# Performance work log

Hardware: AMD Instinct MI355X
Metric: run time of the kernel (lower is better)

## Reference

```python
import jax, jax.numpy as jnp
import numpy as np

NARROW = 127.0                      # narrow int8 range [-127, 127]
ACT_SCALE = 6.0 / 127.0             # fixed stand-in for learned ActQuant per-tensor scale
FLOW_SCALE = 3.96875 / 127.0        # ConstFlowQuant: max_val 3.96875, 8-bit narrow


def ste_round(x):
    # straight-through rounding (Brevitas-style)
    return x + jax.lax.stop_gradient(jnp.round(x) - x)


def act_quant(x, scale):
    # per-tensor narrow int8 fake-quant (quantize -> clamp -> dequantize)
    return scale * jnp.clip(ste_round(x / scale), -NARROW, NARROW)


def weight_quant(w):
    # per-tensor stats-based narrow int8 weight fake-quant
    s = jax.lax.stop_gradient(jnp.max(jnp.abs(w))) / NARROW + 1e-12
    return s * jnp.clip(ste_round(w / s), -NARROW, NARROW)


def conv2d(x, w, b, groups=1, pad=0):
    y = jax.lax.conv_general_dilated(
        x, w, window_strides=(1, 1), padding=[(pad, pad), (pad, pad)],
        dimension_numbers=("NCHW", "OIHW", "NCHW"), feature_group_count=groups)
    return y + b[None, :, None, None]


def setup_inputs() -> dict:
    key = jax.random.key(0)
    ks = jax.random.split(key, 12)
    B, H, W = 8, 120, 160
    cor_planes = 4 * (2 * 3 + 1) ** 2  # 196
    return {
        "flow": jax.random.normal(ks[0], (B, 2, H, W), jnp.float32),
        "corr": jax.random.normal(ks[1], (B, cor_planes, H, W), jnp.float32),
        "Wc1": jax.random.normal(ks[2], (96, cor_planes, 1, 1), jnp.float32) * 0.05,
        "bc1": jax.random.normal(ks[3], (96,), jnp.float32) * 0.05,
        "Wf1": jax.random.normal(ks[4], (64, 2, 1, 1), jnp.float32) * 0.05,
        "bf1": jax.random.normal(ks[5], (64,), jnp.float32) * 0.05,
        "Wf2": jax.random.normal(ks[6], (32, 64, 1, 1), jnp.float32) * 0.05,
        "bf2": jax.random.normal(ks[7], (32,), jnp.float32) * 0.05,
        "Wd": jax.random.normal(ks[8], (128, 1, 3, 3), jnp.float32) * 0.05,
        "bd": jax.random.normal(ks[9], (128,), jnp.float32) * 0.05,
        "Wp": jax.random.normal(ks[10], (80, 128, 1, 1), jnp.float32) * 0.05,
        "bp": jax.random.normal(ks[11], (80,), jnp.float32) * 0.05,
    }


def reference(flow, corr, Wc1, bc1, Wf1, bf1, Wf2, bf2, Wd, bd, Wp, bp):
    # convc1: 1x1 quant conv with output ActQuant, then ReLU
    cor = jax.nn.relu(act_quant(conv2d(corr, weight_quant(Wc1), bc1), ACT_SCALE))
    # convf1: 1x1 quant conv (no output quant), ReLU
    flo = jax.nn.relu(conv2d(flow, weight_quant(Wf1), bf1))
    # convf2: input ActQuant, 1x1 conv, output quant (shared with convc1), ReLU
    flo = jax.nn.relu(act_quant(conv2d(act_quant(flo, ACT_SCALE), weight_quant(Wf2), bf2), ACT_SCALE))
    # QuantCat with ConstFlowQuant on inputs and output -> [B,128,H,W]
    cor_flo = act_quant(
        jnp.concatenate([act_quant(cor, FLOW_SCALE), act_quant(flo, FLOW_SCALE)], axis=1),
        FLOW_SCALE)
    # depthwise 3x3 quant conv (groups=128), input ActQuant
    d = conv2d(act_quant(cor_flo, ACT_SCALE), weight_quant(Wd), bd, groups=128, pad=1)
    # pointwise 1x1 quant conv, input ActQuant, ReLU
    out = jax.nn.relu(conv2d(act_quant(d, ACT_SCALE), weight_quant(Wp), bp))
    # final QuantCat(out, flow) with ConstFlowQuant -> [B,82,H,W]
    return act_quant(
        jnp.concatenate([act_quant(out, FLOW_SCALE), act_quant(flow, FLOW_SCALE)], axis=1),
        FLOW_SCALE)
```

## Files before the change

### kernel.cpp

```cpp
#include <hip/hip_runtime.h>
#include <hip/hip_bf16.h>
#include <cstddef>

#define BB   8
#define HH   120
#define WW   160
#define HW   19200
#define NPIX 153600
#define CORC 196

#define AS_  ((float)(6.0/127.0))
#define FS_  0.03125f

#define OFF_WF1 18832
#define OFF_WF2 18960
#define OFF_WD  21008
#define OFF_WPQ_US 44320
#define CFQ_BYTE_OFF 131072

typedef __attribute__((ext_vector_type(8)))  short short8;
typedef __attribute__((ext_vector_type(4)))  float f32x4;
typedef unsigned int u32;

__device__ __forceinline__ float clip127(float x) {
    return fminf(fmaxf(x, -127.f), 127.f);
}

__device__ __forceinline__ unsigned short f2bf(float x) {
    unsigned int u = __float_as_uint(x);
    unsigned int r = (u + 0x7fffu + ((u >> 16) & 1u)) >> 16;
    return (unsigned short)r;
}

__global__ __launch_bounds__(256) void quant_weights(
    const float* __restrict__ Wc1, const float* __restrict__ Wf1,
    const float* __restrict__ Wf2, const float* __restrict__ Wd,
    const float* __restrict__ Wp,  float* __restrict__ ws)
{
    __shared__ float red[256];
    const int t = blockIdx.x;
    const float* src = (t == 0) ? Wc1 : (t == 1) ? Wf1 : (t == 2) ? Wf2 : (t == 3) ? Wd : Wp;
    const int n = (t == 0) ? 18816 : (t == 1) ? 128 : (t == 2) ? 2048 : (t == 3) ? 1152 : 10240;
    const int tid = threadIdx.x;

    float m = 0.f;
    for (int i = tid; i < n; i += 256) m = fmaxf(m, fabsf(src[i]));
    red[tid] = m;
    __syncthreads();
    for (int s = 128; s > 0; s >>= 1) {
        if (tid < s) red[tid] = fmaxf(red[tid], red[tid + s]);
        __syncthreads();
    }
    const float s = red[0] / 127.0f + 1e-12f;

    if (t == 0) {
        unsigned short* bf = (unsigned short*)ws + 32;
        for (int j = tid; j < 21504; j += 256) {
            const int e    = j & 7;
            const int l    = (j >> 3) & 63;
            const int tile = j >> 9;
            const int nt   = tile % 6;
            const int kt   = tile / 6;
            const int out  = nt * 16 + (l & 15);
            const int k    = kt * 32 + ((l >> 4) << 3) + e;
            float q = 0.f;
            if (k < 196) q = clip127(rintf(Wc1[out * 196 + k] / s));
            bf[j] = f2bf(q);
        }
        if (tid == 0) ws[2] = s;
    } else if (t == 4) {
        unsigned short* bf = (unsigned short*)ws + OFF_WPQ_US;
        for (int j = tid; j < 10240; j += 256) {
            const int e    = j & 7;
            const int l    = (j >> 3) & 63;
            const int tile = j >> 9;
            const int nt   = tile % 5;
            const int kt   = tile / 5;
            const int o    = nt * 16 + (l & 15);
            const int k    = kt * 32 + ((l >> 4) << 3) + e;
            const float q  = clip127(rintf(Wp[o * 128 + k] / s));
            bf[j] = f2bf(q);
        }
        if (tid == 0) ws[1] = s;
    } else {
        for (int i = tid; i < n; i += 256) {
            const float q = clip127(rintf(src[i] / s));
            if (t == 1) {
                ws[OFF_WF1 + i] = s * q;
            } else if (t == 2) {
                int o = i / 64, c = i % 64;
                ws[OFF_WF2 + c * 32 + o] = s * q;
            } else {
                ws[OFF_WD + i] = q;
            }
        }
        if (tid == 0 && t == 3) ws[0] = s;
    }
}

#define TSTRIDE 136
__global__ __launch_bounds__(256, 3) void k1_convc1(
    const float* __restrict__ corr, const float* __restrict__ bc1,
    const float* __restrict__ ws,   signed char* __restrict__ cfq)
{
    __shared__ __align__(1024) char smem[32768];

    const int tid = threadIdx.x;
    const int w   = tid >> 6;
    const int l   = tid & 63;
    const int p0  = blockIdx.x * 128;
    const int b   = p0 / HW;
    const int hw0 = p0 % HW;
    const float* cp = corr + (size_t)b * CORC * HW + hw0;

    const short8* Bfr = (const short8*)((const unsigned short*)ws + 32);

#define STAGE(KT, BASE)                                                               \
    {   _Pragma("unroll")                                                             \
        for (int i = 0; i < 4; ++i) {                                                 \
            const int cl = w * 8 + i * 2;                                             \
            int ch = (KT) * 32 + cl + (l >> 5);                                       \
            ch = ch < CORC ? ch : (CORC - 1);                                         \
            const char* src = (const char*)cp + (size_t)ch * (HW * 4) + ((l & 31) * 16); \
            u32* dst = (u32*)(smem + (BASE) + cl * 512);                              \
            __builtin_amdgcn_global_load_lds(                                         \
                (const __attribute__((address_space(1))) u32*)src,                    \
                (__attribute__((address_space(3))) u32*)dst, 16, 0, 0);               \
        }                                                                             }

    f32x4 a00 = {0.f,0.f,0.f,0.f}, a01 = a00, a02 = a00, a03 = a00, a04 = a00, a05 = a00;
    f32x4 a10 = a00, a11 = a00, a12 = a00, a13 = a00, a14 = a00, a15 = a00;

    STAGE(0, 0)
    STAGE(1, 16384)

    const int pixoff = (w * 32 + (l & 15)) * 4;
    const int chbase = (l >> 4) << 3;

#pragma unroll
    for (int kt = 0; kt < 7; ++kt) {
        const int base = (kt & 1) << 14;

        asm volatile("s_waitcnt vmcnt(4)" ::: "memory");
        __builtin_amdgcn_sched_barrier(0);
        __builtin_amdgcn_s_barrier();
        __builtin_amdgcn_sched_barrier(0);

        float v0[8], v1[8];
#pragma unroll
        for (int e = 0; e < 8; ++e) {
            const char* ap = smem + base + (chbase + e) * 512 + pixoff;
            v0[e] = *(const float*)ap;
            v1[e] = *(const float*)(ap + 64);
        }
        __builtin_amdgcn_sched_barrier(0);
        asm volatile("s_waitcnt lgkmcnt(0)" ::: "memory");
        __builtin_amdgcn_sched_barrier(0);
        __builtin_amdgcn_s_barrier();
        __builtin_amdgcn_sched_barrier(0);

        const short8 b0 = Bfr[(kt * 6 + 0) * 64 + l];
        const short8 b1 = Bfr[(kt * 6 + 1) * 64 + l];
        const short8 b2 = Bfr[(kt * 6 + 2) * 64 + l];
        const short8 b3 = Bfr[(kt * 6 + 3) * 64 + l];
        const short8 b4 = Bfr[(kt * 6 + 4) * 64 + l];
        const short8 b5 = Bfr[(kt * 6 + 5) * 64 + l];
        __builtin_amdgcn_sched_barrier(0);

        if (kt < 5) STAGE(kt + 2, base)
        __builtin_amdgcn_sched_barrier(0);

        short8 h0_, l0_, h1_, l1_;
#pragma unroll
        for (int e = 0; e < 8; ++e) {
            const float va = v0[e], vb = v1[e];
            const unsigned short ha = f2bf(va);
            const unsigned short hb = f2bf(vb);
            h0_[e] = (short)ha; h1_[e] = (short)hb;
            l0_[e] = (short)f2bf(va - __uint_as_float((unsigned int)ha << 16));
            l1_[e] = (short)f2bf(vb - __uint_as_float((unsigned int)hb << 16));
        }

#define MF(BB_, A0, A1)                                                          \
        A0 = __builtin_amdgcn_mfma_f32_16x16x32_bf16(l0_, BB_, A0, 0, 0, 0);     \
        A0 = __builtin_amdgcn_mfma_f32_16x16x32_bf16(h0_, BB_, A0, 0, 0, 0);     \
        A1 = __builtin_amdgcn_mfma_f32_16x16x32_bf16(l1_, BB_, A1, 0, 0, 0);     \
        A1 = __builtin_amdgcn_mfma_f32_16x16x32_bf16(h1_, BB_, A1, 0, 0, 0);
        MF(b0, a00, a10) MF(b1, a01, a11) MF(b2, a02, a12)
        MF(b3, a03, a13) MF(b4, a04, a14) MF(b5, a05, a15)
#undef MF
    }
#undef STAGE

    const float sc1 = ws[2];
    signed char* t8 = (signed char*)smem;

#define EPI(ACC, NT, TILE)                                                        \
    {   const int out = (NT) * 16 + (l & 15);                                     \
        const float bias = bc1[out];                                              \
        _Pragma("unroll")                                                         \
        for (int i = 0; i < 4; ++i) {                                             \
            const int prow = w * 32 + (TILE) * 16 + ((l >> 4) << 2) + i;          \
            float v  = fmaf(sc1, ACC[i], bias);                                   \
            float aq = AS_ * clip127(rintf(v / AS_));                             \
            float r  = fmaxf(aq, 0.f);                                            \
            float kk = fminf(rintf(r * 32.f), 127.f);                             \
            float cf = kk * FS_;                                                  \
            float q8 = clip127(rintf(cf / AS_));                                  \
            t8[out * TSTRIDE + prow] = (signed char)(int)q8;                      \
        }                                                                         }
    EPI(a00, 0, 0) EPI(a01, 1, 0) EPI(a02, 2, 0) EPI(a03, 3, 0) EPI(a04, 4, 0) EPI(a05, 5, 0)
    EPI(a10, 0, 1) EPI(a11, 1, 1) EPI(a12, 2, 1) EPI(a13, 3, 1) EPI(a14, 4, 1) EPI(a15, 5, 1)
#undef EPI
    __syncthreads();

#pragma unroll
    for (int r = 0; r < 12; ++r) {
        const int d   = r * 256 + tid;
        const int out = d >> 5;
        const int pd  = d & 31;
        const unsigned int v = *(const unsigned int*)(t8 + out * TSTRIDE + pd * 4);
        *(unsigned int*)(cfq + (size_t)(b * 128 + out) * HW + hw0 + pd * 4) = v;
    }
}

typedef __attribute__((ext_vector_type(16))) float f32x16;
__global__ __launch_bounds__(256) void k1_flo(
    const float* __restrict__ flow, const float* __restrict__ bf1,
    const float* __restrict__ bf2,  const float* __restrict__ ws,
    signed char* __restrict__ cfq)
{
    const int p  = blockIdx.x * 256 + threadIdx.x;
    const int b  = p / HW;
    const int hw = p % HW;

    const float f0 = flow[(size_t)(b * 2) * HW + hw];
    const float f1 = flow[(size_t)(b * 2 + 1) * HW + hw];

    f32x16 a2a, a2b;
#pragma unroll
    for (int j = 0; j < 16; ++j) { a2a[j] = 0.f; a2b[j] = 0.f; }

    for (int c = 0; c < 64; ++c) {
        const float w0 = ws[OFF_WF1 + 2 * c];
        const float w1 = ws[OFF_WF1 + 2 * c + 1];
        float v  = fmaf(f0, w0, fmaf(f1, w1, bf1[c]));
        float r  = fmaxf(v, 0.f);
        float af = AS_ * fminf(rintf(r / AS_), 127.f);
        const float* w2 = ws + OFF_WF2 + c * 32;
#pragma unroll
        for (int j = 0; j < 16; ++j) {
            a2a[j] = fmaf(af, w2[j],      a2a[j]);
            a2b[j] = fmaf(af, w2[16 + j], a2b[j]);
        }
    }

    signed char* op = cfq + (size_t)b * 128 * HW + (size_t)96 * HW + hw;
#define FLOEPI(ACC, BASE)                                                        \
    _Pragma("unroll")                                                            \
    for (int j = 0; j < 16; ++j) {                                               \
        const int o = (BASE) + j;                                                \
        float v  = ACC[j] + bf2[o];                                              \
        float aq = AS_ * clip127(rintf(v / AS_));                                \
        float r  = fmaxf(aq, 0.f);                                               \
        float kk = fminf(rintf(r * 32.f), 127.f);                                \
        float cf = kk * FS_;                                                     \
        float q8 = clip127(rintf(cf / AS_));                                     \
        op[(size_t)o * HW] = (signed char)(int)q8;                               \
    }
    FLOEPI(a2a, 0) FLOEPI(a2b, 16)
#undef FLOEPI
}

#define STG_STRIDE 44
__global__ __launch_bounds__(256) void k2_dwpw(
    const float* __restrict__ flow, const float* __restrict__ bd,
    const float* __restrict__ bp,   const float* __restrict__ ws,
    const signed char* __restrict__ cfq, float* __restrict__ out)
{
    __shared__ signed char stage[4 * 128 * STG_STRIDE];
    __shared__ unsigned short afrag[64 * 136];

    const int tid = threadIdx.x;
    const int bid = blockIdx.x;
    const int b   = bid / 300;
    const int rem = bid % 300;
    const int h0  = (rem / 5) * 2;
    const int w0  = (rem % 5) * 32;

    for (int j = tid; j < 5120; j += 256) {
        const int i   = j % 10;
        const int c   = (j / 10) % 128;
        const int row = j / 1280;
        const int h   = h0 - 1 + row;
        const int wb  = w0 - 4 + 4 * i;
        unsigned int v = 0u;
        if (h >= 0 && h < HH && wb >= 0 && wb <= WW - 4)
            v = *(const unsigned int*)(cfq + ((size_t)(b * 128 + c) * HW + (size_t)h * WW + wb));
        *(unsigned int*)(stage + (row * 128 + c) * STG_STRIDE + i * 4) = v;
    }
    __syncthreads();

    const int c0 = tid & 63;
    const int pg = tid >> 6;
    const float sd = ws[0], sp = ws[1];
    const float ASsd = AS_ * sd;

    float wd0[9], wd1[9];
#pragma unroll
    for (int t9 = 0; t9 < 9; ++t9) {
        wd0[t9] = ws[OFF_WD + c0 * 9 + t9];
        wd1[t9] = ws[OFF_WD + (c0 + 64) * 9 + t9];
    }
    const float bd0 = bd[c0], bd1 = bd[c0 + 64];

#pragma unroll
    for (int pp = 0; pp < 16; ++pp) {
        const int pix = pg * 16 + pp;
        const int r   = pix >> 5;
        const int col = pix & 31;
        float s0 = 0.f, s1 = 0.f;
#pragma unroll
        for (int dy = 0; dy < 3; ++dy) {
            const int rb = (r + dy) * 128;
            const int xb = 3 + col;
#pragma unroll
            for (int dd = 0; dd < 3; ++dd) {
                s0 = fmaf((float)stage[(rb + c0     ) * STG_STRIDE + xb + dd], wd0[dy * 3 + dd], s0);
                s1 = fmaf((float)stage[(rb + c0 + 64) * STG_STRIDE + xb + dd], wd1[dy * 3 + dd], s1);
            }
        }
        const float q0 = clip127(rintf(fmaf(ASsd, s0, bd0) / AS_));
        const float q1 = clip127(rintf(fmaf(ASsd, s1, bd1) / AS_));
        afrag[pix * 136 + c0]      = f2bf(q0);
        afrag[pix * 136 + c0 + 64] = f2bf(q1);
    }
    __syncthreads();

    const int wv = tid >> 6;
    const int l  = tid & 63;
    const unsigned short* A = afrag + (size_t)(wv * 16 + (l & 15)) * 136 + ((l >> 4) << 3);
    const short8* Bfr = (const short8*)((const unsigned short*)ws + OFF_WPQ_US);

    f32x4 pc0 = {0.f,0.f,0.f,0.f}, pc1 = pc0, pc2 = pc0, pc3 = pc0, pc4 = pc0;

#define PTSTEP(ACC, KT, NT)                                                      \
    {   short8 bq = Bfr[((KT) * 5 + (NT)) * 64 + l];                             \
        ACC = __builtin_amdgcn_mfma_f32_16x16x32_bf16(a_, bq, ACC, 0, 0, 0);     }
#pragma unroll
    for (int kt = 0; kt < 4; ++kt) {
        short8 a_ = *(const short8*)(A + kt * 32);
        PTSTEP(pc0, kt, 0) PTSTEP(pc1, kt, 1) PTSTEP(pc2, kt, 2)
        PTSTEP(pc3, kt, 3) PTSTEP(pc4, kt, 4)
    }
#undef PTSTEP

    const float ASsp = AS_ * sp;
    float* ob = out + (size_t)b * 82 * HW;

#define PEPI(ACC, NT)                                                            \
    {   const int o = (NT) * 16 + (l & 15);                                      \
        const float bias = bp[o];                                                \
        _Pragma("unroll")                                                        \
        for (int i = 0; i < 4; ++i) {                                            \
            const int pix = wv * 16 + ((l >> 4) << 2) + i;                       \
            const int hw  = (h0 + (pix >> 5)) * WW + w0 + (pix & 31);            \
            float v = fmaf(ASsp, ACC[i], bias);                                  \
            float r = fmaxf(v, 0.f);                                             \
            float k = fminf(rintf(r * 32.f), 127.f);                             \
            ob[(size_t)o * HW + hw] = k * FS_;                                   \
        }                                                                        }
    PEPI(pc0, 0) PEPI(pc1, 1) PEPI(pc2, 2) PEPI(pc3, 3) PEPI(pc4, 4)
#undef PEPI

    if (tid < 128) {
        const int ch  = tid >> 6;
        const int pix = tid & 63;
        const int hw  = (h0 + (pix >> 5)) * WW + w0 + (pix & 31);
        const float f = flow[(size_t)(b * 2 + ch) * HW + hw];
        const float k = clip127(rintf(f * 32.f));
        ob[(size_t)(80 + ch) * HW + hw] = k * FS_;
    }
}

extern "C" void kernel_launch(void* const* d_in, const int* in_sizes, int n_in,
                              void* d_out, int out_size, void* d_ws, size_t ws_size,
                              hipStream_t stream) {
    const float* flow = (const float*)d_in[0];
    const float* corr = (const float*)d_in[1];
    const float* Wc1  = (const float*)d_in[2];
    const float* bc1  = (const float*)d_in[3];
    const float* Wf1  = (const float*)d_in[4];
    const float* bf1  = (const float*)d_in[5];
    const float* Wf2  = (const float*)d_in[6];
    const float* bf2  = (const float*)d_in[7];
    const float* Wd   = (const float*)d_in[8];
    const float* bd   = (const float*)d_in[9];
    const float* Wp   = (const float*)d_in[10];
    const float* bp   = (const float*)d_in[11];

    float* ws = (float*)d_ws;
    signed char* cfq = (signed char*)d_ws + CFQ_BYTE_OFF;
    float* out = (float*)d_out;

    quant_weights<<<5, 256, 0, stream>>>(Wc1, Wf1, Wf2, Wd, Wp, ws);
    k1_convc1<<<NPIX / 128, 256, 0, stream>>>(corr, bc1, ws, cfq);
    k1_flo<<<NPIX / 256, 256, 0, stream>>>(flow, bf1, bf2, ws, cfq);
    k2_dwpw<<<2400, 256, 0, stream>>>(flow, bd, bp, ws, cfq, out);
}
```

Before: 158.7 us.

## Give each wave a private LDS slab in convc1 to drop block barriers

The convc1 kernel is restructured so each wave stages its own 32-pixel slab of corr channels into a private double-buffered LDS region. This removes the two per-iteration block-wide barriers and keeps only a vmcnt/lgkmcnt wait. Blocks shrink to 128 threads and 64 pixels, with half the shared memory, to raise occupancy. Block IDs are remapped with an XCD-aware swizzle so consecutive pixel tiles land on the same die. The cost is more, smaller blocks, narrower 128-byte global rows per channel, and a new barrier before the epilogue reuses LDS.

```diff
diff --git a/kernel.cpp b/kernel.cpp
--- a/kernel.cpp
+++ b/kernel.cpp
@@ -98,66 +98,52 @@
     }
 }
 
-#define TSTRIDE 136
-__global__ __launch_bounds__(256, 3) void k1_convc1(
+#define TS8 68
+__global__ __launch_bounds__(128, 4) void k1_convc1(
     const float* __restrict__ corr, const float* __restrict__ bc1,
     const float* __restrict__ ws,   signed char* __restrict__ cfq)
 {
-    __shared__ __align__(1024) char smem[32768];
-
-    const int tid = threadIdx.x;
-    const int w   = tid >> 6;
-    const int l   = tid & 63;
-    const int p0  = blockIdx.x * 128;
-    const int b   = p0 / HW;
-    const int hw0 = p0 % HW;
+    __shared__ __align__(1024) char smem[16384];
+
+    const int tid  = threadIdx.x;
+    const int w    = tid >> 6;
+    const int l    = tid & 63;
+    const int bid  = blockIdx.x;
+    const int wgid = (bid & 7) * 300 + (bid >> 3);
+    const int p0   = wgid * 64;
+    const int b    = p0 / HW;
+    const int hw0  = p0 % HW;
     const float* cp = corr + (size_t)b * CORC * HW + hw0;
 
     const short8* Bfr = (const short8*)((const unsigned short*)ws + 32);
-
-#define STAGE(KT, BASE)                                                               \
-    {   _Pragma("unroll")                                                             \
-        for (int i = 0; i < 4; ++i) {                                                 \
-            const int cl = w * 8 + i * 2;                                             \
-            int ch = (KT) * 32 + cl + (l >> 5);                                       \
-            ch = ch < CORC ? ch : (CORC - 1);                                         \
-            const char* src = (const char*)cp + (size_t)ch * (HW * 4) + ((l & 31) * 16); \
-            u32* dst = (u32*)(smem + (BASE) + cl * 512);                              \
-            __builtin_amdgcn_global_load_lds(                                         \
-                (const __attribute__((address_space(1))) u32*)src,                    \
-                (__attribute__((address_space(3))) u32*)dst, 16, 0, 0);               \
-        }                                                                             }
+    char* slab = smem + w * 8192;
+
+#define STAGE(KT)                                                                  \
+    {   char* dbase = slab + (((KT) & 1) << 12);                                   \
+        _Pragma("unroll")                                                          \
+        for (int i = 0; i < 4; ++i) {                                              \
+            int ch = (KT) * 32 + i * 8 + (l >> 3);                                 \
+            ch = ch < CORC ? ch : (CORC - 1);                                      \
+            const char* src = (const char*)cp + (size_t)ch * (HW * 4)              \
+                              + w * 128 + (l & 7) * 16;                            \
+            u32* dst = (u32*)(dbase + i * 1024);                                   \
+            __builtin_amdgcn_global_load_lds(                                      \
+                (const __attribute__((address_space(1))) u32*)src,                 \
+                (__attribute__((address_space(3))) u32*)dst, 16, 0, 0);            \
+        }                                                                          }
 
     f32x4 a00 = {0.f,0.f,0.f,0.f}, a01 = a00, a02 = a00, a03 = a00, a04 = a00, a05 = a00;
     f32x4 a10 = a00, a11 = a00, a12 = a00, a13 = a00, a14 = a00, a15 = a00;
 
-    STAGE(0, 0)
-    STAGE(1, 16384)
-
-    const int pixoff = (w * 32 + (l & 15)) * 4;
+    STAGE(0)
+    STAGE(1)
+
+    const int pixoff = (l & 15) * 4;
     const int chbase = (l >> 4) << 3;
 
 #pragma unroll
     for (int kt = 0; kt < 7; ++kt) {
-        const int base = (kt & 1) << 14;
-
-        asm volatile("s_waitcnt vmcnt(4)" ::: "memory");
-        __builtin_amdgcn_sched_barrier(0);
-        __builtin_amdgcn_s_barrier();
-        __builtin_amdgcn_sched_barrier(0);
-
-        float v0[8], v1[8];
-#pragma unroll
-        for (int e = 0; e < 8; ++e) {
-            const char* ap = smem + base + (chbase + e) * 512 + pixoff;
-            v0[e] = *(const float*)ap;
-            v1[e] = *(const float*)(ap + 64);
-        }
-        __builtin_amdgcn_sched_barrier(0);
-        asm volatile("s_waitcnt lgkmcnt(0)" ::: "memory");
-        __builtin_amdgcn_sched_barrier(0);
-        __builtin_amdgcn_s_barrier();
-        __builtin_amdgcn_sched_barrier(0);
+        const char* abase = slab + ((kt & 1) << 12);
 
         const short8 b0 = Bfr[(kt * 6 + 0) * 64 + l];
         const short8 b1 = Bfr[(kt * 6 + 1) * 64 + l];
@@ -165,9 +151,21 @@
         const short8 b3 = Bfr[(kt * 6 + 3) * 64 + l];
         const short8 b4 = Bfr[(kt * 6 + 4) * 64 + l];
         const short8 b5 = Bfr[(kt * 6 + 5) * 64 + l];
+
+        asm volatile("s_waitcnt vmcnt(10)" ::: "memory");
         __builtin_amdgcn_sched_barrier(0);
 
-        if (kt < 5) STAGE(kt + 2, base)
+        float v0[8], v1[8];
+#pragma unroll
+        for (int e = 0; e < 8; ++e) {
+            const char* ap = abase + (chbase + e) * 128 + pixoff;
+            v0[e] = *(const float*)ap;
+            v1[e] = *(const float*)(ap + 64);
+        }
+        asm volatile("s_waitcnt lgkmcnt(0)" ::: "memory");
+        __builtin_amdgcn_sched_barrier(0);
+
+        if (kt < 5) STAGE(kt + 2)
         __builtin_amdgcn_sched_barrier(0);
 
         short8 h0_, l0_, h1_, l1_;
@@ -193,6 +191,7 @@
 #undef STAGE
 
     const float sc1 = ws[2];
+    __syncthreads();
     signed char* t8 = (signed char*)smem;
 
 #define EPI(ACC, NT, TILE)                                                        \
@@ -207,7 +206,7 @@
             float kk = fminf(rintf(r * 32.f), 127.f);                             \
             float cf = kk * FS_;                                                  \
             float q8 = clip127(rintf(cf / AS_));                                  \
-            t8[out * TSTRIDE + prow] = (signed char)(int)q8;                      \
+            t8[out * TS8 + prow] = (signed char)(int)q8;                          \
         }                                                                         }
     EPI(a00, 0, 0) EPI(a01, 1, 0) EPI(a02, 2, 0) EPI(a03, 3, 0) EPI(a04, 4, 0) EPI(a05, 5, 0)
     EPI(a10, 0, 1) EPI(a11, 1, 1) EPI(a12, 2, 1) EPI(a13, 3, 1) EPI(a14, 4, 1) EPI(a15, 5, 1)
@@ -216,10 +215,10 @@
 
 #pragma unroll
     for (int r = 0; r < 12; ++r) {
-        const int d   = r * 256 + tid;
-        const int out = d >> 5;
-        const int pd  = d & 31;
-        const unsigned int v = *(const unsigned int*)(t8 + out * TSTRIDE + pd * 4);
+        const int d   = r * 128 + tid;
+        const int out = d >> 4;
+        const int pd  = d & 15;
+        const unsigned int v = *(const unsigned int*)(t8 + out * TS8 + pd * 4);
         *(unsigned int*)(cfq + (size_t)(b * 128 + out) * HW + hw0 + pd * 4) = v;
     }
 }
@@ -404,7 +403,7 @@
     float* out = (float*)d_out;
 
     quant_weights<<<5, 256, 0, stream>>>(Wc1, Wf1, Wf2, Wd, Wp, ws);
-    k1_convc1<<<NPIX / 128, 256, 0, stream>>>(corr, bc1, ws, cfq);
+    k1_convc1<<<NPIX / 64, 128, 0, stream>>>(corr, bc1, ws, cfq);
     k1_flo<<<NPIX / 256, 256, 0, stream>>>(flow, bf1, bf2, ws, cfq);
     k2_dwpw<<<2400, 256, 0, stream>>>(flow, bd, bp, ws, cfq, out);
 }
```

Result: slower. 164.1 us (+3.4%).

## Double convc1 block to 256 pixels with 512 threads and padded LDS slabs

Applied to the files above, without the earlier changes.

The convc1 GEMM kernel now handles 256 pixels per block with 8 waves, so each staged channel row covers 1 KB of contiguous global memory per wave. LDS rows are padded to a 1032-byte stride to cut bank conflicts, and block IDs are remapped so consecutive blocks land on different batches or XCDs. The intent is better global load coalescing and fewer blocks. The cost is twice the LDS per block (about 66 KB), which may limit occupancy.

```diff
diff --git a/kernel.cpp b/kernel.cpp
--- a/kernel.cpp
+++ b/kernel.cpp
@@ -98,19 +98,23 @@
     }
 }
 
-#define TSTRIDE 136
-__global__ __launch_bounds__(256, 3) void k1_convc1(
+#define SLAB 33024
+#define CSTR 1032
+#define TS8  260
+__global__ __launch_bounds__(512, 4) void k1_convc1(
     const float* __restrict__ corr, const float* __restrict__ bc1,
     const float* __restrict__ ws,   signed char* __restrict__ cfq)
 {
-    __shared__ __align__(1024) char smem[32768];
-
-    const int tid = threadIdx.x;
-    const int w   = tid >> 6;
-    const int l   = tid & 63;
-    const int p0  = blockIdx.x * 128;
-    const int b   = p0 / HW;
-    const int hw0 = p0 % HW;
+    __shared__ __align__(1024) char smem[2 * SLAB];
+
+    const int tid  = threadIdx.x;
+    const int w    = tid >> 6;
+    const int l    = tid & 63;
+    const int bid  = blockIdx.x;
+    const int wgid = (bid & 7) * 75 + (bid >> 3);
+    const int p0   = wgid * 256;
+    const int b    = p0 / HW;
+    const int hw0  = p0 % HW;
     const float* cp = corr + (size_t)b * CORC * HW + hw0;
 
     const short8* Bfr = (const short8*)((const unsigned short*)ws + 32);
@@ -118,11 +122,11 @@
 #define STAGE(KT, BASE)                                                               \
     {   _Pragma("unroll")                                                             \
         for (int i = 0; i < 4; ++i) {                                                 \
-            const int cl = w * 8 + i * 2;                                             \
-            int ch = (KT) * 32 + cl + (l >> 5);                                       \
+            const int cl = i * 8 + w;                                                 \
+            int ch = (KT) * 32 + cl;                                                  \
             ch = ch < CORC ? ch : (CORC - 1);                                         \
-            const char* src = (const char*)cp + (size_t)ch * (HW * 4) + ((l & 31) * 16); \
-            u32* dst = (u32*)(smem + (BASE) + cl * 512);                              \
+            const char* src = (const char*)cp + (size_t)ch * (HW * 4) + l * 16;       \
+            u32* dst = (u32*)(smem + (BASE) + cl * CSTR);                             \
             __builtin_amdgcn_global_load_lds(                                         \
                 (const __attribute__((address_space(1))) u32*)src,                    \
                 (__attribute__((address_space(3))) u32*)dst, 16, 0, 0);               \
@@ -132,14 +136,14 @@
     f32x4 a10 = a00, a11 = a00, a12 = a00, a13 = a00, a14 = a00, a15 = a00;
 
     STAGE(0, 0)
-    STAGE(1, 16384)
+    STAGE(1, SLAB)
 
     const int pixoff = (w * 32 + (l & 15)) * 4;
     const int chbase = (l >> 4) << 3;
 
 #pragma unroll
     for (int kt = 0; kt < 7; ++kt) {
-        const int base = (kt & 1) << 14;
+        const int base = (kt & 1) ? SLAB : 0;
 
         asm volatile("s_waitcnt vmcnt(4)" ::: "memory");
         __builtin_amdgcn_sched_barrier(0);
@@ -149,7 +153,7 @@
         float v0[8], v1[8];
 #pragma unroll
         for (int e = 0; e < 8; ++e) {
-            const char* ap = smem + base + (chbase + e) * 512 + pixoff;
+            const char* ap = smem + base + (chbase + e) * CSTR + pixoff;
             v0[e] = *(const float*)ap;
             v1[e] = *(const float*)(ap + 64);
         }
@@ -207,7 +211,7 @@
             float kk = fminf(rintf(r * 32.f), 127.f);                             \
             float cf = kk * FS_;                                                  \
             float q8 = clip127(rintf(cf / AS_));                                  \
-            t8[out * TSTRIDE + prow] = (signed char)(int)q8;                      \
+            t8[out * TS8 + prow] = (signed char)(int)q8;                          \
         }                                                                         }
     EPI(a00, 0, 0) EPI(a01, 1, 0) EPI(a02, 2, 0) EPI(a03, 3, 0) EPI(a04, 4, 0) EPI(a05, 5, 0)
     EPI(a10, 0, 1) EPI(a11, 1, 1) EPI(a12, 2, 1) EPI(a13, 3, 1) EPI(a14, 4, 1) EPI(a15, 5, 1)
@@ -216,11 +220,11 @@
 
 #pragma unroll
     for (int r = 0; r < 12; ++r) {
-        const int d   = r * 256 + tid;
-        const int out = d >> 5;
-        const int pd  = d & 31;
-        const unsigned int v = *(const unsigned int*)(t8 + out * TSTRIDE + pd * 4);
-        *(unsigned int*)(cfq + (size_t)(b * 128 + out) * HW + hw0 + pd * 4) = v;
+        const int d   = r * 512 + tid;
+        const int out = d >> 6;
+        const int pd  = d & 63;
+        const u32 v = *(const u32*)(t8 + out * TS8 + pd * 4);
+        *(u32*)(cfq + (size_t)(b * 128 + out) * HW + hw0 + pd * 4) = v;
     }
 }
 
@@ -404,7 +408,7 @@
     float* out = (float*)d_out;
 
     quant_weights<<<5, 256, 0, stream>>>(Wc1, Wf1, Wf2, Wd, Wp, ws);
-    k1_convc1<<<NPIX / 128, 256, 0, stream>>>(corr, bc1, ws, cfq);
+    k1_convc1<<<NPIX / 256, 512, 0, stream>>>(corr, bc1, ws, cfq);
     k1_flo<<<NPIX / 256, 256, 0, stream>>>(flow, bf1, bf2, ws, cfq);
     k2_dwpw<<<2400, 256, 0, stream>>>(flow, bd, bp, ws, cfq, out);
 }
```

Result: slower. 169.3 us (+6.7%).
